# Kernel optimization log

Measured on AMD Instinct MI355X. Metric: run time of the kernel, lower is better.

## Reference

```python
import jax, jax.numpy as jnp
import numpy as np

N_NODES = 100000
N_EDGES = 800000
N_GRAPHS = 512
D_IN = 128
D_H = 128
N_LAYERS = 3
EPS = 1e-5


def setup_inputs() -> dict:
    key = jax.random.key(0)
    ks = jax.random.split(key, 8)
    x = jax.random.normal(ks[0], (N_NODES, D_IN), dtype=jnp.float32)
    edge_index = jax.random.randint(ks[1], (2, N_EDGES), 0, N_NODES, dtype=jnp.int64)
    batch = jnp.sort(jax.random.randint(ks[2], (N_NODES,), 0, N_GRAPHS, dtype=jnp.int64))
    s = 1.0 / np.sqrt(D_H)
    Ws = jax.random.normal(ks[3], (N_LAYERS, D_H, D_H), dtype=jnp.float32) * s
    bs = jnp.zeros((N_LAYERS, D_H), dtype=jnp.float32)
    gammas = jnp.ones((N_LAYERS, D_H), dtype=jnp.float32)
    betas = jnp.zeros((N_LAYERS, D_H), dtype=jnp.float32)
    W1 = jax.random.normal(ks[4], (D_H, D_H), dtype=jnp.float32) * s
    b1 = jnp.zeros((D_H,), dtype=jnp.float32)
    W2 = jax.random.normal(ks[5], (D_H, 1), dtype=jnp.float32) * s
    b2 = jnp.zeros((1,), dtype=jnp.float32)
    return {"x": x, "edge_index": edge_index, "batch": batch, "Ws": Ws, "bs": bs,
            "gammas": gammas, "betas": betas, "W1": W1, "b1": b1, "W2": W2, "b2": b2}


def reference(x, edge_index, batch, Ws, bs, gammas, betas, W1, b1, W2, b2):
    N = x.shape[0]
    src, dst = edge_index[0], edge_index[1]
    # GCN symmetric norm with self-loops: deg = in-degree + 1 (self loop weight 1)
    deg = jax.ops.segment_sum(jnp.ones_like(dst, dtype=jnp.float32), dst, num_segments=N) + 1.0
    dinv = jax.lax.rsqrt(deg)                      # [N]
    enorm = (dinv[src] * dinv[dst])[:, None]       # [E,1]
    self_w = (1.0 / deg)[:, None]                  # [N,1] self-loop norm dinv_i^2

    h = x
    for l in range(N_LAYERS):
        h = h @ Ws[l]                                                    # linear first (as PyG GCNConv)
        h = jax.ops.segment_sum(enorm * h[src], dst, num_segments=N) + h * self_w
        h = h + bs[l]
        # BatchNorm1d, training-mode per-feature stats (biased variance)
        mu = jnp.mean(h, axis=0)
        var = jnp.mean(jnp.square(h - mu), axis=0)
        h = (h - mu) * jax.lax.rsqrt(var + EPS) * gammas[l] + betas[l]
        h = jax.nn.relu(h)                                               # dropout p=0 -> identity

    # global mean pool over subgraphs
    sums = jax.ops.segment_sum(h, batch, num_segments=N_GRAPHS)
    cnt = jax.ops.segment_sum(jnp.ones((N,), jnp.float32), batch, num_segments=N_GRAPHS)
    Z = sums / jnp.maximum(cnt, 1.0)[:, None]

    # MLP head
    hz = jax.nn.relu(Z @ W1 + b1)
    logits = hz @ W2 + b2                           # [N_GRAPHS, 1]
    return logits
```

## Files before the change

### kernel.cpp

```cpp
#include <hip/hip_runtime.h>
#include <hip/hip_bf16.h>
#include <hip/hip_fp16.h>

#define N_NODES 100000
#define N_EDGES 800000
#define N_GRAPHS 512
#define D 128
#define EPSV 1e-5f

#define NBLK 256
#define EPB  3125
#define NBUK 391
#define MAXB 3072

#define LSTR 68
#define WOFF 4352

#define NSLOT 256

typedef _Float16 half8 __attribute__((ext_vector_type(8)));
typedef float floatx16 __attribute__((ext_vector_type(16)));

__device__ __forceinline__ float relu_f(float x){ return fmaxf(x, 0.0f); }

__device__ __forceinline__ void scan512(int* sd, int t)
{
    for (int off = 1; off < 512; off <<= 1){
        int i2 = t + 256;
        int v1 = (t  >= off) ? sd[t  - off] : 0;
        int v2 = (i2 >= off) ? sd[i2 - off] : 0;
        __syncthreads();
        sd[t]  += v1;
        sd[i2] += v2;
        __syncthreads();
    }
}

__global__ __launch_bounds__(256) void k_front(const int* __restrict__ dst,
                                               int* __restrict__ blockHist,
                                               const float* __restrict__ Ws,
                                               unsigned int* __restrict__ wpack,
                                               unsigned int* __restrict__ zbase,
                                               int zn,
                                               const int* __restrict__ batch,
                                               int* __restrict__ gstart,
                                               int* __restrict__ row_ptr)
{
    __shared__ int h[NBUK];
    int j = blockIdx.x, t = threadIdx.x;
    if (j < NBLK){
        for (int u = t; u < NBUK; u += 256) h[u] = 0;
        __syncthreads();
        int e0 = j * EPB;
        for (int e = e0 + t; e < e0 + EPB; e += 256)
            atomicAdd(&h[dst[e] >> 8], 1);
        __syncthreads();
        for (int u = t; u < NBUK; u += 256) blockHist[j * NBUK + u] = h[u];
    } else {
        int b = j - NBLK;
        int idx = b * 256 + t;
        if (idx == 0){
            row_ptr[N_NODES] = N_EDGES;
            gstart[N_GRAPHS] = N_NODES;
        }
        if (idx < 3 * 128 * 64){
            int l  = idx >> 13;
            int r  = idx & 8191;
            int c  = r >> 6;
            int k2 = r & 63;
            const float* W = Ws + l * D * D;
            __half2 hh = __floats2half2_rn(W[(size_t)(2 * k2) * D + c],
                                           W[(size_t)(2 * k2 + 1) * D + c]);
            wpack[idx] = *(unsigned int*)&hh;
        }
        int stride = 96 * 256;
        for (int i = idx; i < zn; i += stride) zbase[i] = 0u;
        if (idx < N_GRAPHS){
            int g = idx;
            int lo = 0, hi = N_NODES;
            while (lo < hi){ int m = (lo + hi) >> 1; if (batch[m] < g) lo = m + 1; else hi = m; }
            gstart[g] = lo;
        }
    }
}

__global__ __launch_bounds__(256) void k_p2a(const int* __restrict__ blockHist,
                                             int* __restrict__ colScan,
                                             int* __restrict__ bucketTotal)
{
    __shared__ int sd[256];
    int b = blockIdx.x, t = threadIdx.x;
    int v = blockHist[t * NBUK + b];
    sd[t] = v;
    __syncthreads();
    for (int off = 1; off < 256; off <<= 1){
        int u = (t >= off) ? sd[t - off] : 0;
        __syncthreads();
        sd[t] += u;
        __syncthreads();
    }
    colScan[t * NBUK + b] = sd[t] - v;
    if (t == 255) bucketTotal[b] = sd[255];
}

__global__ __launch_bounds__(256) void k_p3(const int* __restrict__ src,
                                            const int* __restrict__ dst,
                                            const int* __restrict__ colScan,
                                            const int* __restrict__ bucketTotal,
                                            int2* __restrict__ ebuf)
{
    __shared__ int sd[512];
    __shared__ int cur[NBUK];
    int j = blockIdx.x, t = threadIdx.x;
    int i2 = t + 256;
    sd[t]  = (t  < NBUK) ? bucketTotal[t]  : 0;
    sd[i2] = (i2 < NBUK) ? bucketTotal[i2] : 0;
    __syncthreads();
    scan512(sd, t);
    if (t < NBUK)
        cur[t]  = (sd[t]  - bucketTotal[t])  + colScan[j * NBUK + t];
    if (i2 < NBUK)
        cur[i2] = (sd[i2] - bucketTotal[i2]) + colScan[j * NBUK + i2];
    __syncthreads();
    int e0 = j * EPB;
    for (int e = e0 + t; e < e0 + EPB; e += 256){
        int s = src[e], d = dst[e];
        int pos = atomicAdd(&cur[d >> 8], 1);
        int2 v; v.x = s; v.y = d;
        ebuf[pos] = v;
    }
}

__global__ __launch_bounds__(256) void k_p4(const int2* __restrict__ ebuf,
                                            const int* __restrict__ bucketTotal,
                                            int* __restrict__ row_ptr,
                                            int* __restrict__ csr_src,
                                            float* __restrict__ dinv,
                                            float* __restrict__ selfw)
{
    __shared__ int2 stash[MAXB];
    __shared__ int sdScan[512];
    __shared__ int bins[256];
    __shared__ int sd[256];
    int b = blockIdx.x, t = threadIdx.x;
    int i2 = t + 256;
    sdScan[t]  = (t  < NBUK) ? bucketTotal[t]  : 0;
    sdScan[i2] = (i2 < NBUK) ? bucketTotal[i2] : 0;
    __syncthreads();
    scan512(sdScan, t);
    int cntb = bucketTotal[b];
    int base = sdScan[b] - cntb;
    bool st = (cntb <= MAXB);
    bins[t] = 0;
    __syncthreads();
    for (int i = t; i < cntb; i += 256){
        int2 ed = ebuf[base + i];
        if (st) stash[i] = ed;
        atomicAdd(&bins[ed.y & 255], 1);
    }
    __syncthreads();
    int a0 = bins[t];
    sd[t] = a0;
    __syncthreads();
    for (int off = 1; off < 256; off <<= 1){
        int v = (t >= off) ? sd[t - off] : 0;
        __syncthreads();
        sd[t] += v;
        __syncthreads();
    }
    int pex = sd[t] - a0;
    int node = b * 256 + t;
    if (node < N_NODES){
        row_ptr[node] = base + pex;
        float d = (float)(a0 + 1);
        dinv[node]  = rsqrtf(d);
        selfw[node] = 1.0f / d;
    }
    __syncthreads();
    bins[t] = pex;
    __syncthreads();
    for (int i = t; i < cntb; i += 256){
        int2 ed = st ? stash[i] : ebuf[base + i];
        int pos = atomicAdd(&bins[ed.y & 255], 1);
        csr_src[base + pos] = ed.x;
    }
}

__global__ __launch_bounds__(256) void k_gemm(const float* __restrict__ A,
                                              const unsigned int* __restrict__ wp,
                                              const float* __restrict__ scale,
                                              const float* __restrict__ shift,
                                              __half* __restrict__ outh,
                                              int useBn)
{
    __shared__ unsigned int lds32[WOFF + 128 * LSTR];
    int tid = threadIdx.x;
    int rowBase = blockIdx.x * 64;

    #pragma unroll
    for (int rep = 0; rep < 8; rep++){
        int f  = rep * 256 + tid;
        int m  = f >> 5;
        int c4 = f & 31;
        int row = rowBase + m;
        if (row >= N_NODES) row = N_NODES - 1;
        float4 v = *(const float4*)(A + (size_t)row * D + c4 * 4);
        if (useBn){
            float4 sc = *(const float4*)(scale + c4 * 4);
            float4 sh = *(const float4*)(shift + c4 * 4);
            v.x = relu_f(fmaf(v.x, sc.x, sh.x));
            v.y = relu_f(fmaf(v.y, sc.y, sh.y));
            v.z = relu_f(fmaf(v.z, sc.z, sh.z));
            v.w = relu_f(fmaf(v.w, sc.w, sh.w));
        }
        __half2 h0 = __floats2half2_rn(v.x, v.y);
        __half2 h1 = __floats2half2_rn(v.z, v.w);
        uint2 u; u.x = *(unsigned int*)&h0; u.y = *(unsigned int*)&h1;
        *(uint2*)&lds32[m * LSTR + 2 * c4] = u;
    }
    {
        const uint4* gw = (const uint4*)wp;
        #pragma unroll
        for (int rep = 0; rep < 8; rep++){
            int f = rep * 256 + tid;
            int c = f >> 4;
            int q = f & 15;
            uint4 v = gw[f];
            *(uint4*)&lds32[WOFF + c * LSTR + 4 * q] = v;
        }
    }
    __syncthreads();

    int lane = tid & 63, wv = tid >> 6;
    int quad = lane >> 5;
    int ml   = (lane & 31) + (wv & 1) * 32;
    int cA   = (wv >> 1) * 64;
    int c0   = cA + (lane & 31);
    int c1   = c0 + 32;
    const unsigned int* aRow  = lds32 + ml * LSTR;
    const unsigned int* bRow0 = lds32 + WOFF + c0 * LSTR;
    const unsigned int* bRow1 = lds32 + WOFF + c1 * LSTR;
    floatx16 acc0 = {};
    floatx16 acc1 = {};
    #pragma unroll
    for (int ch = 0; ch < 8; ch++){
        int o = ch * 8 + quad * 4;
        half8 af = *(const half8*)(aRow  + o);
        half8 b0 = *(const half8*)(bRow0 + o);
        half8 b1 = *(const half8*)(bRow1 + o);
        acc0 = __builtin_amdgcn_mfma_f32_32x32x16_f16(af, b0, acc0, 0, 0, 0);
        acc1 = __builtin_amdgcn_mfma_f32_32x32x16_f16(af, b1, acc1, 0, 0, 0);
    }
    int rBase = rowBase + (wv & 1) * 32 + 4 * quad;
    #pragma unroll
    for (int r = 0; r < 16; r++){
        int outRow = rBase + (r & 3) + 8 * (r >> 2);
        if (outRow < N_NODES){
            outh[(size_t)outRow * D + c0] = __float2half(acc0[r]);
            outh[(size_t)outRow * D + c1] = __float2half(acc1[r]);
        }
    }
}

__global__ __launch_bounds__(256) void k_agg(const __half* __restrict__ t,
                                             const int* __restrict__ row_ptr,
                                             const int* __restrict__ csr_src,
                                             const float* __restrict__ dinv,
                                             const float* __restrict__ selfw,
                                             const float* __restrict__ bias,
                                             float* __restrict__ outb,
                                             float* __restrict__ Spart,
                                             float* __restrict__ Qpart)
{
    __shared__ float ldsS[4][128];
    __shared__ float ldsQ[4][128];
    int lane = threadIdx.x & 63;
    int wv   = threadIdx.x >> 6;
    int i = blockIdx.x * 4 + wv;
    const __half2* t2 = (const __half2*)t;
    int p0 = row_ptr[i], p1 = row_ptr[i + 1];
    float sw = selfw[i];
    float dvi = dinv[i];
    float2 a = __half22float2(t2[(size_t)i * 64 + lane]);
    float ax = a.x * sw, ay = a.y * sw;
    int p = p0;
    for (; p + 8 <= p1; p += 8){
        int s[8]; float wv8[8];
        #pragma unroll
        for (int j = 0; j < 8; j++){ s[j] = csr_src[p + j]; }
        #pragma unroll
        for (int j = 0; j < 8; j++){ wv8[j] = dinv[s[j]] * dvi; }
        __half2 v[8];
        #pragma unroll
        for (int j = 0; j < 8; j++) v[j] = t2[(size_t)s[j] * 64 + lane];
        #pragma unroll
        for (int j = 0; j < 8; j++){
            float2 f = __half22float2(v[j]);
            ax = fmaf(wv8[j], f.x, ax);
            ay = fmaf(wv8[j], f.y, ay);
        }
    }
    for (; p + 4 <= p1; p += 4){
        int s0 = csr_src[p], s1 = csr_src[p+1], s2 = csr_src[p+2], s3 = csr_src[p+3];
        float w0 = dinv[s0] * dvi, w1 = dinv[s1] * dvi;
        float w2 = dinv[s2] * dvi, w3 = dinv[s3] * dvi;
        float2 v0 = __half22float2(t2[(size_t)s0 * 64 + lane]);
        float2 v1 = __half22float2(t2[(size_t)s1 * 64 + lane]);
        float2 v2 = __half22float2(t2[(size_t)s2 * 64 + lane]);
        float2 v3 = __half22float2(t2[(size_t)s3 * 64 + lane]);
        ax = fmaf(w0, v0.x, ax); ay = fmaf(w0, v0.y, ay);
        ax = fmaf(w1, v1.x, ax); ay = fmaf(w1, v1.y, ay);
        ax = fmaf(w2, v2.x, ax); ay = fmaf(w2, v2.y, ay);
        ax = fmaf(w3, v3.x, ax); ay = fmaf(w3, v3.y, ay);
    }
    for (; p < p1; ++p){
        int s = csr_src[p];
        float w = dinv[s] * dvi;
        float2 v = __half22float2(t2[(size_t)s * 64 + lane]);
        ax = fmaf(w, v.x, ax);
        ay = fmaf(w, v.y, ay);
    }
    float2 b2 = ((const float2*)bias)[lane];
    ax += b2.x; ay += b2.y;
    float2 o; o.x = ax; o.y = ay;
    ((float2*)outb)[(size_t)i * 64 + lane] = o;
    ldsS[wv][2 * lane] = ax;       ldsS[wv][2 * lane + 1] = ay;
    ldsQ[wv][2 * lane] = ax * ax;  ldsQ[wv][2 * lane + 1] = ay * ay;
    __syncthreads();
    int tid = threadIdx.x;
    int slotBase = (blockIdx.x & (NSLOT - 1)) * 128;
    if (tid < 128){
        float s = ldsS[0][tid] + ldsS[1][tid] + ldsS[2][tid] + ldsS[3][tid];
        atomicAdd(&Spart[slotBase + tid], s);
    } else {
        int f = tid - 128;
        float q = ldsQ[0][f] + ldsQ[1][f] + ldsQ[2][f] + ldsQ[3][f];
        atomicAdd(&Qpart[slotBase + f], q);
    }
}

__global__ __launch_bounds__(256) void k_fin2(const float* __restrict__ Spart,
                                              const float* __restrict__ Qpart,
                                              const float* __restrict__ gamma,
                                              const float* __restrict__ beta,
                                              float* __restrict__ sc,
                                              float* __restrict__ sh)
{
    int t = threadIdx.x;
    int f = t & 127;
    const float* src = (t < 128) ? Spart : Qpart;
    float acc = 0.f;
    for (int s2 = 0; s2 < NSLOT; s2++)
        acc += src[s2 * 128 + f];
    __shared__ float red[256];
    red[t] = acc;
    __syncthreads();
    if (t < 128){
        float Sv = red[t];
        float Qv = red[t + 128];
        float mean = Sv * (1.0f / N_NODES);
        float var  = fmaxf(Qv * (1.0f / N_NODES) - mean * mean, 0.0f);
        float inv  = rsqrtf(var + EPSV);
        float gm = gamma[f] * inv;
        sc[f] = gm;
        sh[f] = beta[f] - mean * gm;
    }
}

__global__ __launch_bounds__(256) void k_tail(const float* __restrict__ h,
                                              const int* __restrict__ gstart,
                                              const float* __restrict__ sc,
                                              const float* __restrict__ sh,
                                              const float* __restrict__ W1,
                                              const float* __restrict__ b1,
                                              const float* __restrict__ W2,
                                              const float* __restrict__ b2,
                                              float* __restrict__ out)
{
    __shared__ float part[256];
    __shared__ float z[128];
    __shared__ float red[128];
    int g = blockIdx.x;
    int tid = threadIdx.x;
    int f = tid & 127;
    int hf = tid >> 7;
    int s0 = gstart[g], s1 = gstart[g + 1];
    float scv = sc[f], shv = sh[f];
    float acc = 0.f;
    for (int i = s0 + hf; i < s1; i += 2)
        acc += relu_f(fmaf(h[(size_t)i * D + f], scv, shv));
    part[tid] = acc;
    __syncthreads();
    if (tid < 128){
        float c = fmaxf((float)(s1 - s0), 1.0f);
        z[f] = (part[f] + part[f + 128]) / c;
    }
    __syncthreads();
    float a = 0.f;
    int k0 = hf * 64;
    #pragma unroll 8
    for (int k = k0; k < k0 + 64; k++)
        a = fmaf(z[k], W1[k * D + f], a);
    part[tid] = a;
    __syncthreads();
    if (tid < 128){
        float av = relu_f(part[f] + part[f + 128] + b1[f]);
        red[f] = av * W2[f];
    }
    __syncthreads();
    for (int s2 = 64; s2 > 0; s2 >>= 1){
        if (tid < s2) red[tid] += red[tid + s2];
        __syncthreads();
    }
    if (tid == 0) out[g] = red[0] + b2[0];
}

extern "C" void kernel_launch(void* const* d_in, const int* in_sizes, int n_in,
                              void* d_out, int out_size, void* d_ws, size_t ws_size,
                              hipStream_t stream)
{
    const float* x      = (const float*)d_in[0];
    const int*   ei     = (const int*)d_in[1];
    const int*   batch  = (const int*)d_in[2];
    const float* Ws     = (const float*)d_in[3];
    const float* bs     = (const float*)d_in[4];
    const float* gammas = (const float*)d_in[5];
    const float* betas  = (const float*)d_in[6];
    const float* W1     = (const float*)d_in[7];
    const float* b1     = (const float*)d_in[8];
    const float* W2     = (const float*)d_in[9];
    const float* b2     = (const float*)d_in[10];
    float* out = (float*)d_out;

    const int* src = ei;
    const int* dst = ei + N_EDGES;

    char* w = (char*)d_ws;
    size_t off = 0;
    auto alloc = [&](size_t bytes) -> void* {
        void* p = w + off;
        off += (bytes + 255) & ~(size_t)255;
        return p;
    };
    int*   row_ptr     = (int*)  alloc((size_t)(N_NODES + 1) * 4);
    float* dinv        = (float*)alloc((size_t)N_NODES * 4);
    float* selfw       = (float*)alloc((size_t)N_NODES * 4);
    int*   csr_src     = (int*)  alloc((size_t)N_EDGES * 4);
    int*   blockHist   = (int*)  alloc((size_t)NBLK * NBUK * 4);
    int*   colScan     = (int*)  alloc((size_t)NBLK * NBUK * 4);
    int*   bucketTotal = (int*)  alloc((size_t)NBUK * 4);
    unsigned int* wpack = (unsigned int*)alloc((size_t)3 * 128 * 64 * 4);
    int*   gstart      = (int*)  alloc((size_t)(N_GRAPHS + 1) * 4);
    size_t zoff = off;
    float* stats       = (float*)alloc((size_t)3 * 2 * NSLOT * 128 * 4);
    size_t zend = off;
    float* ssh         = (float*)alloc(3 * 256 * 4);
    __half* tbuf       = (__half*)alloc((size_t)N_NODES * 128 * 2);
    float* hbuf        = (float*)alloc((size_t)N_NODES * 128 * 4);
    if (off > ws_size) return;

    int2* ebuf = (int2*)tbuf;

    k_front<<<NBLK + 96, 256, 0, stream>>>(dst, blockHist, Ws, wpack,
                                           (unsigned int*)(w + zoff),
                                           (int)((zend - zoff) >> 2),
                                           batch, gstart, row_ptr);
    k_p2a<<<NBUK, 256, 0, stream>>>(blockHist, colScan, bucketTotal);
    k_p3 <<<NBLK, 256, 0, stream>>>(src, dst, colScan, bucketTotal, ebuf);
    k_p4 <<<NBUK, 256, 0, stream>>>(ebuf, bucketTotal, row_ptr, csr_src, dinv, selfw);

    const float* curIn = x;
    for (int l = 0; l < 3; l++){
        float* Sp = stats + (size_t)l * 2 * NSLOT * 128;
        float* Qp = Sp + NSLOT * 128;
        k_gemm<<<(N_NODES + 63) / 64, 256, 0, stream>>>(
            curIn, wpack + l * 8192,
            l ? ssh + (l - 1) * 256       : nullptr,
            l ? ssh + (l - 1) * 256 + 128 : nullptr,
            tbuf, l ? 1 : 0);
        k_agg<<<25000, 256, 0, stream>>>(
            tbuf, row_ptr, csr_src, dinv, selfw,
            bs + l * 128, hbuf, Sp, Qp);
        k_fin2<<<1, 256, 0, stream>>>(
            Sp, Qp, gammas + l * 128, betas + l * 128,
            ssh + l * 256, ssh + l * 256 + 128);
        curIn = hbuf;
    }

    k_tail<<<N_GRAPHS, 256, 0, stream>>>(hbuf, gstart,
                                         ssh + 2 * 256, ssh + 2 * 256 + 128,
                                         W1, b1, W2, b2, out);
}
```

Measured before the change: 414.0 us.

## Fold source-side GCN norm into GEMM epilogue and widen aggregation gathers

The GEMM epilogue now multiplies each output row by dinv of that row, so aggregation becomes a plain sum of neighbour rows followed by one multiply by the destination's dinv. This removes the per-edge dinv[src] gather and the separate selfw array. The aggregation kernel is restructured so 16 lanes handle one node with 16-byte (8-half) gathers, each wave covering 8 nodes, and per-block stats are reduced with shuffles before the atomics. Stat slots are halved to shrink the final reduction. Pre-scaling in fp16 slightly changes rounding.

```diff
diff --git a/kernel.cpp b/kernel.cpp
--- a/kernel.cpp
+++ b/kernel.cpp
@@ -16,7 +16,7 @@
 #define LSTR 68
 #define WOFF 4352
 
-#define NSLOT 256
+#define NSLOT 128
 
 typedef _Float16 half8 __attribute__((ext_vector_type(8)));
 typedef float floatx16 __attribute__((ext_vector_type(16)));
@@ -135,8 +135,7 @@
                                             const int* __restrict__ bucketTotal,
                                             int* __restrict__ row_ptr,
                                             int* __restrict__ csr_src,
-                                            float* __restrict__ dinv,
-                                            float* __restrict__ selfw)
+                                            float* __restrict__ dinv)
 {
     __shared__ int2 stash[MAXB];
     __shared__ int sdScan[512];
@@ -174,7 +173,6 @@
         row_ptr[node] = base + pex;
         float d = (float)(a0 + 1);
         dinv[node]  = rsqrtf(d);
-        selfw[node] = 1.0f / d;
     }
     __syncthreads();
     bins[t] = pex;
@@ -190,6 +188,7 @@
                                               const unsigned int* __restrict__ wp,
                                               const float* __restrict__ scale,
                                               const float* __restrict__ shift,
+                                              const float* __restrict__ dinv,
                                               __half* __restrict__ outh,
                                               int useBn)
 {
@@ -256,17 +255,27 @@
     for (int r = 0; r < 16; r++){
         int outRow = rBase + (r & 3) + 8 * (r >> 2);
         if (outRow < N_NODES){
-            outh[(size_t)outRow * D + c0] = __float2half(acc0[r]);
-            outh[(size_t)outRow * D + c1] = __float2half(acc1[r]);
-        }
-    }
+            float dv = dinv[outRow];
+            outh[(size_t)outRow * D + c0] = __float2half(acc0[r] * dv);
+            outh[(size_t)outRow * D + c1] = __float2half(acc1[r] * dv);
+        }
+    }
+}
+
+__device__ __forceinline__ void accum8(float* acc, uint4 v)
+{
+    float2 f0 = __half22float2(*(__half2*)&v.x);
+    float2 f1 = __half22float2(*(__half2*)&v.y);
+    float2 f2 = __half22float2(*(__half2*)&v.z);
+    float2 f3 = __half22float2(*(__half2*)&v.w);
+    acc[0] += f0.x; acc[1] += f0.y; acc[2] += f1.x; acc[3] += f1.y;
+    acc[4] += f2.x; acc[5] += f2.y; acc[6] += f3.x; acc[7] += f3.y;
 }
 
 __global__ __launch_bounds__(256) void k_agg(const __half* __restrict__ t,
                                              const int* __restrict__ row_ptr,
                                              const int* __restrict__ csr_src,
                                              const float* __restrict__ dinv,
-                                             const float* __restrict__ selfw,
                                              const float* __restrict__ bias,
                                              float* __restrict__ outb,
                                              float* __restrict__ Spart,
@@ -274,68 +283,91 @@
 {
     __shared__ float ldsS[4][128];
     __shared__ float ldsQ[4][128];
-    int lane = threadIdx.x & 63;
-    int wv   = threadIdx.x >> 6;
-    int i = blockIdx.x * 4 + wv;
-    const __half2* t2 = (const __half2*)t;
-    int p0 = row_ptr[i], p1 = row_ptr[i + 1];
-    float sw = selfw[i];
-    float dvi = dinv[i];
-    float2 a = __half22float2(t2[(size_t)i * 64 + lane]);
-    float ax = a.x * sw, ay = a.y * sw;
-    int p = p0;
-    for (; p + 8 <= p1; p += 8){
-        int s[8]; float wv8[8];
+    int tid  = threadIdx.x;
+    int lane = tid & 63;
+    int wv   = tid >> 6;
+    int q    = lane & 15;
+    int g    = lane >> 4;
+    const uint4* t4 = (const uint4*)t;
+    float4* out4 = (float4*)outb;
+
+    float4 bia = ((const float4*)bias)[2 * q];
+    float4 bib = ((const float4*)bias)[2 * q + 1];
+
+    float sa[8] = {0.f,0.f,0.f,0.f,0.f,0.f,0.f,0.f};
+    float qa[8] = {0.f,0.f,0.f,0.f,0.f,0.f,0.f,0.f};
+
+    int i0 = blockIdx.x * 32 + wv * 8 + g * 2;
+
+    for (int n = 0; n < 2; n++){
+        int i  = i0 + n;
+        int p  = row_ptr[i];
+        int pe = row_ptr[i + 1];
+        float acc[8];
+        {
+            uint4 v = t4[(size_t)i * 16 + q];
+            float2 f0 = __half22float2(*(__half2*)&v.x);
+            float2 f1 = __half22float2(*(__half2*)&v.y);
+            float2 f2 = __half22float2(*(__half2*)&v.z);
+            float2 f3 = __half22float2(*(__half2*)&v.w);
+            acc[0] = f0.x; acc[1] = f0.y; acc[2] = f1.x; acc[3] = f1.y;
+            acc[4] = f2.x; acc[5] = f2.y; acc[6] = f3.x; acc[7] = f3.y;
+        }
+        for (; p + 4 <= pe; p += 4){
+            int s0 = csr_src[p],     s1 = csr_src[p + 1];
+            int s2 = csr_src[p + 2], s3 = csr_src[p + 3];
+            uint4 v0 = t4[(size_t)s0 * 16 + q];
+            uint4 v1 = t4[(size_t)s1 * 16 + q];
+            uint4 v2 = t4[(size_t)s2 * 16 + q];
+            uint4 v3 = t4[(size_t)s3 * 16 + q];
+            accum8(acc, v0); accum8(acc, v1); accum8(acc, v2); accum8(acc, v3);
+        }
+        for (; p < pe; ++p){
+            int s = csr_src[p];
+            uint4 v = t4[(size_t)s * 16 + q];
+            accum8(acc, v);
+        }
+        float dvi = dinv[i];
+        acc[0] = fmaf(acc[0], dvi, bia.x);
+        acc[1] = fmaf(acc[1], dvi, bia.y);
+        acc[2] = fmaf(acc[2], dvi, bia.z);
+        acc[3] = fmaf(acc[3], dvi, bia.w);
+        acc[4] = fmaf(acc[4], dvi, bib.x);
+        acc[5] = fmaf(acc[5], dvi, bib.y);
+        acc[6] = fmaf(acc[6], dvi, bib.z);
+        acc[7] = fmaf(acc[7], dvi, bib.w);
+        out4[(size_t)i * 32 + 2 * q]     = make_float4(acc[0], acc[1], acc[2], acc[3]);
+        out4[(size_t)i * 32 + 2 * q + 1] = make_float4(acc[4], acc[5], acc[6], acc[7]);
         #pragma unroll
-        for (int j = 0; j < 8; j++){ s[j] = csr_src[p + j]; }
+        for (int k = 0; k < 8; k++){
+            sa[k] += acc[k];
+            qa[k]  = fmaf(acc[k], acc[k], qa[k]);
+        }
+    }
+
+    #pragma unroll
+    for (int k = 0; k < 8; k++){
+        sa[k] += __shfl_xor(sa[k], 16);
+        sa[k] += __shfl_xor(sa[k], 32);
+        qa[k] += __shfl_xor(qa[k], 16);
+        qa[k] += __shfl_xor(qa[k], 32);
+    }
+    if (g == 0){
         #pragma unroll
-        for (int j = 0; j < 8; j++){ wv8[j] = dinv[s[j]] * dvi; }
-        __half2 v[8];
-        #pragma unroll
-        for (int j = 0; j < 8; j++) v[j] = t2[(size_t)s[j] * 64 + lane];
-        #pragma unroll
-        for (int j = 0; j < 8; j++){
-            float2 f = __half22float2(v[j]);
-            ax = fmaf(wv8[j], f.x, ax);
-            ay = fmaf(wv8[j], f.y, ay);
-        }
-    }
-    for (; p + 4 <= p1; p += 4){
-        int s0 = csr_src[p], s1 = csr_src[p+1], s2 = csr_src[p+2], s3 = csr_src[p+3];
-        float w0 = dinv[s0] * dvi, w1 = dinv[s1] * dvi;
-        float w2 = dinv[s2] * dvi, w3 = dinv[s3] * dvi;
-        float2 v0 = __half22float2(t2[(size_t)s0 * 64 + lane]);
-        float2 v1 = __half22float2(t2[(size_t)s1 * 64 + lane]);
-        float2 v2 = __half22float2(t2[(size_t)s2 * 64 + lane]);
-        float2 v3 = __half22float2(t2[(size_t)s3 * 64 + lane]);
-        ax = fmaf(w0, v0.x, ax); ay = fmaf(w0, v0.y, ay);
-        ax = fmaf(w1, v1.x, ax); ay = fmaf(w1, v1.y, ay);
-        ax = fmaf(w2, v2.x, ax); ay = fmaf(w2, v2.y, ay);
-        ax = fmaf(w3, v3.x, ax); ay = fmaf(w3, v3.y, ay);
-    }
-    for (; p < p1; ++p){
-        int s = csr_src[p];
-        float w = dinv[s] * dvi;
-        float2 v = __half22float2(t2[(size_t)s * 64 + lane]);
-        ax = fmaf(w, v.x, ax);
-        ay = fmaf(w, v.y, ay);
-    }
-    float2 b2 = ((const float2*)bias)[lane];
-    ax += b2.x; ay += b2.y;
-    float2 o; o.x = ax; o.y = ay;
-    ((float2*)outb)[(size_t)i * 64 + lane] = o;
-    ldsS[wv][2 * lane] = ax;       ldsS[wv][2 * lane + 1] = ay;
-    ldsQ[wv][2 * lane] = ax * ax;  ldsQ[wv][2 * lane + 1] = ay * ay;
-    __syncthreads();
-    int tid = threadIdx.x;
+        for (int k = 0; k < 8; k++){
+            ldsS[wv][8 * q + k] = sa[k];
+            ldsQ[wv][8 * q + k] = qa[k];
+        }
+    }
+    __syncthreads();
     int slotBase = (blockIdx.x & (NSLOT - 1)) * 128;
     if (tid < 128){
         float s = ldsS[0][tid] + ldsS[1][tid] + ldsS[2][tid] + ldsS[3][tid];
         atomicAdd(&Spart[slotBase + tid], s);
     } else {
         int f = tid - 128;
-        float q = ldsQ[0][f] + ldsQ[1][f] + ldsQ[2][f] + ldsQ[3][f];
-        atomicAdd(&Qpart[slotBase + f], q);
+        float qv = ldsQ[0][f] + ldsQ[1][f] + ldsQ[2][f] + ldsQ[3][f];
+        atomicAdd(&Qpart[slotBase + f], qv);
     }
 }
 
@@ -444,7 +476,6 @@
     };
     int*   row_ptr     = (int*)  alloc((size_t)(N_NODES + 1) * 4);
     float* dinv        = (float*)alloc((size_t)N_NODES * 4);
-    float* selfw       = (float*)alloc((size_t)N_NODES * 4);
     int*   csr_src     = (int*)  alloc((size_t)N_EDGES * 4);
     int*   blockHist   = (int*)  alloc((size_t)NBLK * NBUK * 4);
     int*   colScan     = (int*)  alloc((size_t)NBLK * NBUK * 4);
@@ -467,7 +498,7 @@
                                            batch, gstart, row_ptr);
     k_p2a<<<NBUK, 256, 0, stream>>>(blockHist, colScan, bucketTotal);
     k_p3 <<<NBLK, 256, 0, stream>>>(src, dst, colScan, bucketTotal, ebuf);
-    k_p4 <<<NBUK, 256, 0, stream>>>(ebuf, bucketTotal, row_ptr, csr_src, dinv, selfw);
+    k_p4 <<<NBUK, 256, 0, stream>>>(ebuf, bucketTotal, row_ptr, csr_src, dinv);
 
     const float* curIn = x;
     for (int l = 0; l < 3; l++){
@@ -477,9 +508,9 @@
             curIn, wpack + l * 8192,
             l ? ssh + (l - 1) * 256       : nullptr,
             l ? ssh + (l - 1) * 256 + 128 : nullptr,
-            tbuf, l ? 1 : 0);
-        k_agg<<<25000, 256, 0, stream>>>(
-            tbuf, row_ptr, csr_src, dinv, selfw,
+            dinv, tbuf, l ? 1 : 0);
+        k_agg<<<N_NODES / 32, 256, 0, stream>>>(
+            tbuf, row_ptr, csr_src, dinv,
             bs + l * 128, hbuf, Sp, Qp);
         k_fin2<<<1, 256, 0, stream>>>(
             Sp, Qp, gammas + l * 128, betas + l * 128,
```

Measured after the change: 375.5 us. -9.3%, faster.
